# Optimization experiments

Hardware: AMD Instinct MI355X
Metric: run time of the kernel (lower is better)

Reference implementation:

```python
import jax, jax.numpy as jnp
import numpy as np

BS = 128      # batch
L = 512       # encoder sequence length
ENC = 512     # enc_hs
DEC = 1024    # dec_hs
ATTN = 512    # attn_sz
EMB = 256     # emb_sz
VOCAB = 128   # alphabet_size
MAX_LEN = 128 # text_max_len
SOS = 0


def setup_inputs() -> dict:
    key = jax.random.key(0)
    ks = jax.random.split(key, 10)
    s = 0.02
    return {
        "enc_out": jax.random.normal(ks[0], (BS, ENC, L), jnp.float32),
        # attention.encoder_conv (Conv1d enc->attn, kernel 1 == matmul)
        "W_enc": jax.random.normal(ks[1], (ATTN, ENC), jnp.float32) * s,
        "b_enc": jnp.zeros((ATTN,), jnp.float32),
        # attention.decoder_linear
        "W_dec": jax.random.normal(ks[2], (ATTN, DEC), jnp.float32) * s,
        "b_dec": jnp.zeros((ATTN,), jnp.float32),
        # attention.energy_layer (Conv1d attn->1, kernel 1)
        "v_e": jax.random.normal(ks[3], (ATTN,), jnp.float32) * s,
        "b_e": jnp.zeros((), jnp.float32),
        # embedding table
        "emb_table": jax.random.normal(ks[4], (VOCAB, EMB), jnp.float32) * s,
        # LSTM (single layer), PyTorch gate order i,f,g,o
        "W_ih": jax.random.normal(ks[5], (4 * DEC, EMB + ENC), jnp.float32) * s,
        "W_hh": jax.random.normal(ks[6], (4 * DEC, DEC), jnp.float32) * s,
        "b_ih": jnp.zeros((4 * DEC,), jnp.float32),
        "b_hh": jnp.zeros((4 * DEC,), jnp.float32),
        # output projection
        "W_out": jax.random.normal(ks[7], (VOCAB, DEC), jnp.float32) * s,
        "b_out": jnp.zeros((VOCAB,), jnp.float32),
    }


def reference(enc_out, W_enc, b_enc, W_dec, b_dec, v_e, b_e, emb_table,
              W_ih, W_hh, b_ih, b_hh, W_out, b_out):
    bs = enc_out.shape[0]
    # encoder_conv applied once: [bs, attn, L]
    weighted_enc = jnp.einsum('ae,bel->bal', W_enc, enc_out) + b_enc[None, :, None]

    def step(carry, _):
        x_idx, h, c = carry
        emb_x = emb_table[x_idx]                                   # [bs, emb]
        # Bahdanau attention
        wdec = h @ W_dec.T + b_dec                                 # [bs, attn]
        pre = jnp.tanh(weighted_enc + wdec[:, :, None])            # [bs, attn, L]
        scores = jnp.einsum('bal,a->bl', pre, v_e) + b_e           # [bs, L]
        alphas = jax.nn.softmax(scores, axis=-1)                   # [bs, L]
        context = jnp.einsum('bel,bl->be', enc_out, alphas)        # [bs, enc]
        # LSTM cell (PyTorch gate order i, f, g, o)
        rnn_x = jnp.concatenate([emb_x, context], axis=1)          # [bs, emb+enc]
        gates = rnn_x @ W_ih.T + b_ih + h @ W_hh.T + b_hh          # [bs, 4*dec]
        i, f, g, o = jnp.split(gates, 4, axis=1)
        i = jax.nn.sigmoid(i); f = jax.nn.sigmoid(f)
        g = jnp.tanh(g); o = jax.nn.sigmoid(o)
        c_new = f * c + i * g
        h_new = o * jnp.tanh(c_new)
        logits = h_new @ W_out.T + b_out                           # [bs, vocab]
        logp = jax.nn.log_softmax(logits, axis=-1)
        next_word = jnp.argmax(logp, axis=1).astype(jnp.int32)
        return (next_word, h_new, c_new), (logp, next_word, alphas)

    x0 = jnp.full((bs,), SOS, dtype=jnp.int32)
    h0 = jnp.zeros((bs, DEC), enc_out.dtype)
    c0 = jnp.zeros((bs, DEC), enc_out.dtype)
    _, (logp, preds, attn) = jax.lax.scan(step, (x0, h0, c0), None, length=MAX_LEN)
    # [T,bs,*] -> [bs,T,*]
    return logp.transpose(1, 0, 2), preds.transpose(1, 0), attn.transpose(1, 0, 2)
```

## Files before the change

### kernel.cpp

```cpp
#include <hip/hip_runtime.h>
#include <math.h>

#define BS 128
#define L 512
#define ENC 512
#define DEC 1024
#define ATTN 512
#define EMB 256
#define VOCAB 128
#define TMAX 128
#define KCAT 1792
#define G4 4096

#define OFF_WET    0ull
#define OFF_WGR    33554432ull
#define OFF_BGR    40894464ull
#define OFF_WOUTT  40898560ull
#define OFF_WDT    41029632ull
#define OFF_C      41553920ull
#define OFF_XCAT   41816064ull
#define OFF_GPART  42045440ull

__device__ __forceinline__ float tanh_fast(float x) {
    float ax = fabsf(x);
    float e = __expf(-2.f * ax);
    float d = 1.f + e;
    float r = __builtin_amdgcn_rcpf(d);
    r = r * (2.f - d * r);
    float t = 1.f - 2.f * e * r;
    return copysignf(t, x);
}

__global__ void k_prep(const float* __restrict__ W_ih, const float* __restrict__ W_hh,
                       const float* __restrict__ b_ih, const float* __restrict__ b_hh,
                       const float* __restrict__ W_out, const float* __restrict__ W_dec,
                       float* __restrict__ Wgr, float* __restrict__ bgr,
                       float* __restrict__ WoutT, float* __restrict__ WdT) {
    long i = (long)blockIdx.x * 256 + threadIdx.x;
    if (i < (long)G4 * KCAT) {
        int mp = (int)(i / KCAT), k = (int)(i % KCAT);
        int d = mp >> 2, g = mp & 3;
        int r = g * DEC + d;
        Wgr[i] = (k < EMB + ENC) ? W_ih[(long)r * (EMB + ENC) + k]
                                 : W_hh[(long)r * DEC + (k - (EMB + ENC))];
        return;
    }
    long j = i - (long)G4 * KCAT;
    if (j < G4) {
        int d = (int)(j >> 2), g = (int)(j & 3);
        int r = g * DEC + d;
        bgr[j] = b_ih[r] + b_hh[r];
        return;
    }
    long m = j - G4;
    if (m < (long)DEC * VOCAB) {
        int k = (int)(m / VOCAB), v = (int)(m % VOCAB);
        WoutT[m] = W_out[(long)v * DEC + k];
        return;
    }
    long p = m - (long)DEC * VOCAB;
    if (p < (long)DEC * ATTN) {
        int k = (int)(p / ATTN), a = (int)(p % ATTN);
        WdT[p] = W_dec[(long)a * DEC + k];
    }
}

__global__ void k_init(const float* __restrict__ emb_table,
                       float* __restrict__ c, float* __restrict__ Xcat) {
    long i = (long)blockIdx.x * 256 + threadIdx.x;
    if (i < BS * DEC) { c[i] = 0.f; return; }
    long j = i - BS * DEC;
    if (j < (long)BS * KCAT) {
        int cdx = (int)(j % KCAT);
        Xcat[j] = (cdx < EMB) ? emb_table[cdx] : 0.f;
    }
}

__global__ __launch_bounds__(256) void k_wenc(const float* __restrict__ W_enc,
                                              const float* __restrict__ b_enc,
                                              const float* __restrict__ enc_out,
                                              float* __restrict__ weT) {
    __shared__ float As[16][68];
    __shared__ float Bs[16][68];
    int b = blockIdx.z;
    int a0 = blockIdx.y * 64;
    int l0 = blockIdx.x * 64;
    int t = threadIdx.x;
    int ty = t >> 4, tx = t & 15;
    float acc[4][4] = {};
    for (int e0 = 0; e0 < ENC; e0 += 16) {
        {
            int ar = t >> 2;
            int kg = (t & 3) << 2;
            float4 w4 = *(const float4*)&W_enc[(size_t)(a0 + ar) * ENC + e0 + kg];
            As[kg + 0][ar] = w4.x; As[kg + 1][ar] = w4.y; As[kg + 2][ar] = w4.z; As[kg + 3][ar] = w4.w;
            int er = t >> 4;
            int lg = (t & 15) << 2;
            float4 x4 = *(const float4*)&enc_out[((size_t)b * ENC + e0 + er) * L + l0 + lg];
            *(float4*)&Bs[er][lg] = x4;
        }
        __syncthreads();
        #pragma unroll
        for (int kk = 0; kk < 16; kk++) {
            float4 a4 = *(const float4*)&As[kk][ty * 4];
            float4 x4 = *(const float4*)&Bs[kk][tx * 4];
            float av[4] = {a4.x, a4.y, a4.z, a4.w};
            float xv[4] = {x4.x, x4.y, x4.z, x4.w};
            #pragma unroll
            for (int i = 0; i < 4; i++)
                #pragma unroll
                for (int j = 0; j < 4; j++) acc[i][j] += av[i] * xv[j];
        }
        __syncthreads();
    }
    float be0 = b_enc[a0 + ty * 4 + 0];
    float be1 = b_enc[a0 + ty * 4 + 1];
    float be2 = b_enc[a0 + ty * 4 + 2];
    float be3 = b_enc[a0 + ty * 4 + 3];
    #pragma unroll
    for (int j = 0; j < 4; j++) {
        int l = l0 + tx * 4 + j;
        float4 o = {acc[0][j] + be0, acc[1][j] + be1, acc[2][j] + be2, acc[3][j] + be3};
        *(float4*)&weT[((size_t)b * L + l) * ATTN + a0 + ty * 4] = o;
    }
}

__global__ __launch_bounds__(512) void k_ao(const float* __restrict__ gpart,
                                            const float* __restrict__ bgr,
                                            const float* __restrict__ WoutT,
                                            const float* __restrict__ b_out,
                                            const float* __restrict__ emb_table,
                                            const float* __restrict__ WdT,
                                            const float* __restrict__ b_dec,
                                            float* __restrict__ c,
                                            float* __restrict__ logp_out,
                                            float* __restrict__ preds_out,
                                            float* __restrict__ Xcat,
                                            const float* __restrict__ weT,
                                            const float* __restrict__ v_e,
                                            const float* __restrict__ b_e,
                                            const float* __restrict__ enc_out,
                                            float* __restrict__ attn_out, int ts) {
    __shared__ float hs[DEC];
    __shared__ float wd[ATTN];
    __shared__ float ve[ATTN];
    __shared__ float al[L];
    __shared__ float red[512];
    __shared__ float rv[128];
    __shared__ int ri[128];
    int b = blockIdx.x;
    int t = threadIdx.x;

    if (ts > 0) {
        #pragma unroll
        for (int q = 0; q < 2; q++) {
            int d = q * 512 + t;
            const float* gp = gpart + (size_t)b * G4 + d * 4;
            float4 g = *(const float4*)gp;
            #pragma unroll
            for (int ks = 1; ks < 4; ks++) {
                float4 p = *(const float4*)(gp + (size_t)ks * BS * G4);
                g.x += p.x; g.y += p.y; g.z += p.z; g.w += p.w;
            }
            float4 bb = *(const float4*)&bgr[(size_t)d * 4];
            float gi = g.x + bb.x, gf = g.y + bb.y, gg = g.z + bb.z, go = g.w + bb.w;
            float fi = 1.f / (1.f + expf(-gi));
            float ff = 1.f / (1.f + expf(-gf));
            float fg = tanhf(gg);
            float fo = 1.f / (1.f + expf(-go));
            size_t ix = (size_t)b * DEC + d;
            float cn = ff * c[ix] + fi * fg;
            float hn = fo * tanhf(cn);
            c[ix] = cn;
            hs[d] = hn;
            Xcat[(size_t)b * KCAT + EMB + ENC + d] = hn;
        }
        __syncthreads();
        int v = t & 127, kh = t >> 7;
        const float* wp = WoutT + (size_t)kh * 256 * VOCAB + v;
        float acc = 0.f;
        #pragma unroll 8
        for (int k = 0; k < 256; k++) acc += wp[(size_t)k * VOCAB] * hs[kh * 256 + k];
        red[t] = acc;
        __syncthreads();
        float logits = 0.f;
        if (t < 128) {
            logits = ((red[t] + red[t + 128]) + (red[t + 256] + red[t + 384])) + b_out[t];
            rv[t] = logits; ri[t] = t;
        }
        __syncthreads();
        for (int s = 64; s; s >>= 1) {
            if (t < s) {
                float ov = rv[t + s]; int oi = ri[t + s];
                if (ov > rv[t] || (ov == rv[t] && oi < ri[t])) { rv[t] = ov; ri[t] = oi; }
            }
            __syncthreads();
        }
        float m = rv[0]; int am = ri[0];
        __syncthreads();
        if (t < 128) red[t] = expf(logits - m);
        __syncthreads();
        for (int s = 64; s; s >>= 1) { if (t < s && t + s < 128) red[t] += red[t + s]; __syncthreads(); }
        if (t < 128) logp_out[((size_t)b * TMAX + (ts - 1)) * VOCAB + t] = logits - m - logf(red[0]);
        if (t == 0) preds_out[(size_t)b * TMAX + (ts - 1)] = (float)am;
        if (t < 256) Xcat[(size_t)b * KCAT + t] = emb_table[(size_t)am * EMB + t];
        {
            const float* wdp = WdT + t;
            float s = 0.f;
            #pragma unroll 16
            for (int k = 0; k < DEC; k++) s += wdp[(size_t)k * ATTN] * hs[k];
            wd[t] = s + b_dec[t];
        }
        if (ts == TMAX) return;
    } else {
        wd[t] = b_dec[t];
    }
    ve[t] = v_e[t];
    __syncthreads();

    const float* row = weT + ((size_t)b * L + t) * ATTN;
    float acc = 0.f;
    #pragma unroll 8
    for (int a4 = 0; a4 < ATTN; a4 += 4) {
        float4 x = *(const float4*)&row[a4];
        acc += ve[a4 + 0] * tanh_fast(x.x + wd[a4 + 0]);
        acc += ve[a4 + 1] * tanh_fast(x.y + wd[a4 + 1]);
        acc += ve[a4 + 2] * tanh_fast(x.z + wd[a4 + 2]);
        acc += ve[a4 + 3] * tanh_fast(x.w + wd[a4 + 3]);
    }
    float sc = acc + b_e[0];
    red[t] = sc;
    __syncthreads();
    for (int s = 256; s; s >>= 1) { if (t < s) red[t] = fmaxf(red[t], red[t + s]); __syncthreads(); }
    float m = red[0];
    __syncthreads();
    float e = expf(sc - m);
    red[t] = e;
    __syncthreads();
    for (int s = 256; s; s >>= 1) { if (t < s) red[t] += red[t + s]; __syncthreads(); }
    float inv = 1.f / red[0];
    al[t] = e * inv;
    __syncthreads();
    attn_out[((size_t)b * TMAX + ts) * L + t] = al[t];
    const float* erow = enc_out + ((size_t)b * ENC + t) * L;
    float cacc = 0.f;
    #pragma unroll 8
    for (int l4 = 0; l4 < L; l4 += 4) {
        float4 x = *(const float4*)&erow[l4];
        float4 a4 = *(const float4*)&al[l4];
        cacc += x.x * a4.x + x.y * a4.y + x.z * a4.z + x.w * a4.w;
    }
    Xcat[(size_t)b * KCAT + EMB + t] = cacc;
}

__global__ __launch_bounds__(256) void k_gates(const float* __restrict__ Wgr,
                                               const float* __restrict__ Xcat,
                                               float* __restrict__ gates_part) {
    __shared__ float As[16][68];
    __shared__ float Xs[16][36];
    int M0 = blockIdx.x * 64;
    int b0 = blockIdx.y * 32;
    int ks = blockIdx.z;
    int kbase = ks * 448, kend = kbase + 448;
    int t = threadIdx.x, ty = t >> 4, tx = t & 15;
    int r = t >> 2, kg = (t & 3) << 2;
    float acc[4][2] = {};
    float4 wreg = *(const float4*)&Wgr[(size_t)(M0 + r) * KCAT + kbase + kg];
    float4 xreg;
    if (t < 128) xreg = *(const float4*)&Xcat[(size_t)(b0 + r) * KCAT + kbase + kg];
    for (int k0 = kbase; k0 < kend; k0 += 16) {
        As[kg + 0][r] = wreg.x; As[kg + 1][r] = wreg.y; As[kg + 2][r] = wreg.z; As[kg + 3][r] = wreg.w;
        if (t < 128) {
            Xs[kg + 0][r] = xreg.x; Xs[kg + 1][r] = xreg.y; Xs[kg + 2][r] = xreg.z; Xs[kg + 3][r] = xreg.w;
        }
        __syncthreads();
        if (k0 + 16 < kend) {
            wreg = *(const float4*)&Wgr[(size_t)(M0 + r) * KCAT + k0 + 16 + kg];
            if (t < 128) xreg = *(const float4*)&Xcat[(size_t)(b0 + r) * KCAT + k0 + 16 + kg];
        }
        #pragma unroll
        for (int kk = 0; kk < 16; kk++) {
            float4 a4 = *(const float4*)&As[kk][ty * 4];
            float xb0 = Xs[kk][tx * 2], xb1 = Xs[kk][tx * 2 + 1];
            acc[0][0] += a4.x * xb0; acc[0][1] += a4.x * xb1;
            acc[1][0] += a4.y * xb0; acc[1][1] += a4.y * xb1;
            acc[2][0] += a4.z * xb0; acc[2][1] += a4.z * xb1;
            acc[3][0] += a4.w * xb0; acc[3][1] += a4.w * xb1;
        }
        __syncthreads();
    }
    float* gp = gates_part + (size_t)ks * BS * G4;
    #pragma unroll
    for (int j = 0; j < 2; j++) {
        float4 o = {acc[0][j], acc[1][j], acc[2][j], acc[3][j]};
        *(float4*)&gp[(size_t)(b0 + tx * 2 + j) * G4 + M0 + ty * 4] = o;
    }
}

extern "C" void kernel_launch(void* const* d_in, const int* in_sizes, int n_in,
                              void* d_out, int out_size, void* d_ws, size_t ws_size,
                              hipStream_t stream) {
    const float* enc_out = (const float*)d_in[0];
    const float* W_enc   = (const float*)d_in[1];
    const float* b_enc   = (const float*)d_in[2];
    const float* W_dec   = (const float*)d_in[3];
    const float* b_dec   = (const float*)d_in[4];
    const float* v_e     = (const float*)d_in[5];
    const float* b_e     = (const float*)d_in[6];
    const float* emb     = (const float*)d_in[7];
    const float* W_ih    = (const float*)d_in[8];
    const float* W_hh    = (const float*)d_in[9];
    const float* b_ih    = (const float*)d_in[10];
    const float* b_hh    = (const float*)d_in[11];
    const float* W_out   = (const float*)d_in[12];
    const float* b_out   = (const float*)d_in[13];

    float* ws    = (float*)d_ws;
    float* weT   = ws + OFF_WET;
    float* Wgr   = ws + OFF_WGR;
    float* bgr   = ws + OFF_BGR;
    float* WoutT = ws + OFF_WOUTT;
    float* WdT   = ws + OFF_WDT;
    float* c     = ws + OFF_C;
    float* Xcat  = ws + OFF_XCAT;
    float* gpart = ws + OFF_GPART;

    float* logp_out  = (float*)d_out;
    float* preds_out = logp_out + (size_t)BS * TMAX * VOCAB;
    float* attn_out  = preds_out + (size_t)BS * TMAX;

    {
        long n = (long)G4 * KCAT + G4 + (long)DEC * VOCAB + (long)DEC * ATTN;
        k_prep<<<(int)((n + 255) / 256), 256, 0, stream>>>(W_ih, W_hh, b_ih, b_hh, W_out, W_dec,
                                                           Wgr, bgr, WoutT, WdT);
    }
    {
        long n = (long)BS * DEC + (long)BS * KCAT;
        k_init<<<(int)((n + 255) / 256), 256, 0, stream>>>(emb, c, Xcat);
    }
    k_wenc<<<dim3(8, 8, 128), 256, 0, stream>>>(W_enc, b_enc, enc_out, weT);

    for (int t = 0; t < TMAX; t++) {
        k_ao<<<128, 512, 0, stream>>>(gpart, bgr, WoutT, b_out, emb, WdT, b_dec, c,
                                      logp_out, preds_out, Xcat, weT, v_e, b_e,
                                      enc_out, attn_out, t);
        k_gates<<<dim3(64, 4, 4), 256, 0, stream>>>(Wgr, Xcat, gpart);
    }
    k_ao<<<128, 512, 0, stream>>>(gpart, bgr, WoutT, b_out, emb, WdT, b_dec, c,
                                  logp_out, preds_out, Xcat, weT, v_e, b_e,
                                  enc_out, attn_out, TMAX);
}
```

Measured before the change: 22.07 ms.

## Split per-batch attention step across two blocks with pairwise global-flag sync

The per-step attention/output kernel now launches two blocks per batch row instead of one. Each block computes half of the attention scores and half of the context vector, exchanging scores through global memory. The two blocks coordinate with an atomic counter spin barrier, and the old cell state is read before the first barrier so one block can overwrite it safely. The aim is to double the number of active CUs during the memory-bound attention phase, at the cost of redundant LSTM/W_dec work in both blocks and inter-block spin synchronisation that assumes co-residency.

```diff
diff --git a/kernel.cpp b/kernel.cpp
--- a/kernel.cpp
+++ b/kernel.cpp
@@ -18,6 +18,8 @@
 #define OFF_WOUTT  40898560ull
 #define OFF_WDT    41029632ull
 #define OFF_C      41553920ull
+#define OFF_SC     41684992ull
+#define OFF_FLAG   41750528ull
 #define OFF_XCAT   41816064ull
 #define OFF_GPART  42045440ull
 
@@ -29,6 +31,19 @@
     r = r * (2.f - d * r);
     float t = 1.f - 2.f * e * r;
     return copysignf(t, x);
+}
+
+__device__ __forceinline__ void pairsync(int* flag, int target) {
+    __syncthreads();
+    if (threadIdx.x == 0) {
+        __threadfence();
+        __hip_atomic_fetch_add(flag, 1, __ATOMIC_ACQ_REL, __HIP_MEMORY_SCOPE_AGENT);
+        while (__hip_atomic_load(flag, __ATOMIC_RELAXED, __HIP_MEMORY_SCOPE_AGENT) < target) {
+            __builtin_amdgcn_s_sleep(4);
+        }
+        __threadfence();
+    }
+    __syncthreads();
 }
 
 __global__ void k_prep(const float* __restrict__ W_ih, const float* __restrict__ W_hh,
@@ -66,8 +81,10 @@
 }
 
 __global__ void k_init(const float* __restrict__ emb_table,
-                       float* __restrict__ c, float* __restrict__ Xcat) {
+                       float* __restrict__ c, float* __restrict__ Xcat,
+                       int* __restrict__ flags) {
     long i = (long)blockIdx.x * 256 + threadIdx.x;
+    if (i < BS * 16) flags[i] = 0;
     if (i < BS * DEC) { c[i] = 0.f; return; }
     long j = i - BS * DEC;
     if (j < (long)BS * KCAT) {
@@ -125,22 +142,24 @@
     }
 }
 
-__global__ __launch_bounds__(512) void k_ao(const float* __restrict__ gpart,
-                                            const float* __restrict__ bgr,
-                                            const float* __restrict__ WoutT,
-                                            const float* __restrict__ b_out,
-                                            const float* __restrict__ emb_table,
-                                            const float* __restrict__ WdT,
-                                            const float* __restrict__ b_dec,
-                                            float* __restrict__ c,
-                                            float* __restrict__ logp_out,
-                                            float* __restrict__ preds_out,
-                                            float* __restrict__ Xcat,
-                                            const float* __restrict__ weT,
-                                            const float* __restrict__ v_e,
-                                            const float* __restrict__ b_e,
-                                            const float* __restrict__ enc_out,
-                                            float* __restrict__ attn_out, int ts) {
+__global__ __launch_bounds__(512) void k_aof(const float* __restrict__ gpart,
+                                             const float* __restrict__ bgr,
+                                             const float* __restrict__ WoutT,
+                                             const float* __restrict__ b_out,
+                                             const float* __restrict__ emb_table,
+                                             const float* __restrict__ WdT,
+                                             const float* __restrict__ b_dec,
+                                             float* __restrict__ c,
+                                             float* __restrict__ logp_out,
+                                             float* __restrict__ preds_out,
+                                             float* __restrict__ Xcat,
+                                             const float* __restrict__ weT,
+                                             const float* __restrict__ v_e,
+                                             const float* __restrict__ b_e,
+                                             const float* __restrict__ enc_out,
+                                             float* __restrict__ attn_out,
+                                             float* __restrict__ sc_g,
+                                             int* __restrict__ flags, int ts) {
     __shared__ float hs[DEC];
     __shared__ float wd[ATTN];
     __shared__ float ve[ATTN];
@@ -148,10 +167,16 @@
     __shared__ float red[512];
     __shared__ float rv[128];
     __shared__ int ri[128];
-    int b = blockIdx.x;
+    __shared__ float scl[256];
+    int b = blockIdx.x >> 1, h = blockIdx.x & 1;
     int t = threadIdx.x;
+    int* flag = flags + b * 16;
+    int msync = (ts == 0) ? 0 : (2 * ts - 1);
 
     if (ts > 0) {
+        float cold0 = c[(size_t)b * DEC + t];
+        float cold1 = c[(size_t)b * DEC + 512 + t];
+        pairsync(flag, 2 * (++msync));
         #pragma unroll
         for (int q = 0; q < 2; q++) {
             int d = q * 512 + t;
@@ -168,42 +193,46 @@
             float ff = 1.f / (1.f + expf(-gf));
             float fg = tanhf(gg);
             float fo = 1.f / (1.f + expf(-go));
-            size_t ix = (size_t)b * DEC + d;
-            float cn = ff * c[ix] + fi * fg;
+            float cold = q ? cold1 : cold0;
+            float cn = ff * cold + fi * fg;
             float hn = fo * tanhf(cn);
-            c[ix] = cn;
+            if (h == 0) {
+                c[(size_t)b * DEC + d] = cn;
+                Xcat[(size_t)b * KCAT + EMB + ENC + d] = hn;
+            }
             hs[d] = hn;
-            Xcat[(size_t)b * KCAT + EMB + ENC + d] = hn;
         }
         __syncthreads();
-        int v = t & 127, kh = t >> 7;
-        const float* wp = WoutT + (size_t)kh * 256 * VOCAB + v;
-        float acc = 0.f;
-        #pragma unroll 8
-        for (int k = 0; k < 256; k++) acc += wp[(size_t)k * VOCAB] * hs[kh * 256 + k];
-        red[t] = acc;
-        __syncthreads();
-        float logits = 0.f;
-        if (t < 128) {
-            logits = ((red[t] + red[t + 128]) + (red[t + 256] + red[t + 384])) + b_out[t];
-            rv[t] = logits; ri[t] = t;
-        }
-        __syncthreads();
-        for (int s = 64; s; s >>= 1) {
-            if (t < s) {
-                float ov = rv[t + s]; int oi = ri[t + s];
-                if (ov > rv[t] || (ov == rv[t] && oi < ri[t])) { rv[t] = ov; ri[t] = oi; }
+        if (h == 0) {
+            int v = t & 127, kh = t >> 7;
+            const float* wp = WoutT + (size_t)kh * 256 * VOCAB + v;
+            float acc = 0.f;
+            #pragma unroll 8
+            for (int k = 0; k < 256; k++) acc += wp[(size_t)k * VOCAB] * hs[kh * 256 + k];
+            red[t] = acc;
+            __syncthreads();
+            float logits = 0.f;
+            if (t < 128) {
+                logits = ((red[t] + red[t + 128]) + (red[t + 256] + red[t + 384])) + b_out[t];
+                rv[t] = logits; ri[t] = t;
             }
             __syncthreads();
-        }
-        float m = rv[0]; int am = ri[0];
-        __syncthreads();
-        if (t < 128) red[t] = expf(logits - m);
-        __syncthreads();
-        for (int s = 64; s; s >>= 1) { if (t < s && t + s < 128) red[t] += red[t + s]; __syncthreads(); }
-        if (t < 128) logp_out[((size_t)b * TMAX + (ts - 1)) * VOCAB + t] = logits - m - logf(red[0]);
-        if (t == 0) preds_out[(size_t)b * TMAX + (ts - 1)] = (float)am;
-        if (t < 256) Xcat[(size_t)b * KCAT + t] = emb_table[(size_t)am * EMB + t];
+            for (int s = 64; s; s >>= 1) {
+                if (t < s) {
+                    float ov = rv[t + s]; int oi = ri[t + s];
+                    if (ov > rv[t] || (ov == rv[t] && oi < ri[t])) { rv[t] = ov; ri[t] = oi; }
+                }
+                __syncthreads();
+            }
+            float m = rv[0]; int am = ri[0];
+            __syncthreads();
+            if (t < 128) red[t] = expf(logits - m);
+            __syncthreads();
+            for (int s = 64; s; s >>= 1) { if (t < s && t + s < 128) red[t] += red[t + s]; __syncthreads(); }
+            if (t < 128) logp_out[((size_t)b * TMAX + (ts - 1)) * VOCAB + t] = logits - m - logf(red[0]);
+            if (t == 0) preds_out[(size_t)b * TMAX + (ts - 1)] = (float)am;
+            if (t < 256) Xcat[(size_t)b * KCAT + t] = emb_table[(size_t)am * EMB + t];
+        }
         {
             const float* wdp = WdT + t;
             float s = 0.f;
@@ -218,17 +247,32 @@
     ve[t] = v_e[t];
     __syncthreads();
 
-    const float* row = weT + ((size_t)b * L + t) * ATTN;
-    float acc = 0.f;
-    #pragma unroll 8
-    for (int a4 = 0; a4 < ATTN; a4 += 4) {
-        float4 x = *(const float4*)&row[a4];
-        acc += ve[a4 + 0] * tanh_fast(x.x + wd[a4 + 0]);
-        acc += ve[a4 + 1] * tanh_fast(x.y + wd[a4 + 1]);
-        acc += ve[a4 + 2] * tanh_fast(x.z + wd[a4 + 2]);
-        acc += ve[a4 + 3] * tanh_fast(x.w + wd[a4 + 3]);
-    }
-    float sc = acc + b_e[0];
+    {
+        int r2 = t >> 1, ah = t & 1;
+        int l = h * 256 + r2;
+        const float* row = weT + ((size_t)b * L + l) * ATTN + ah * 256;
+        float acc = 0.f;
+        #pragma unroll 8
+        for (int a4 = 0; a4 < 256; a4 += 4) {
+            float4 x = *(const float4*)&row[a4];
+            int a = ah * 256 + a4;
+            acc += ve[a + 0] * tanh_fast(x.x + wd[a + 0]);
+            acc += ve[a + 1] * tanh_fast(x.y + wd[a + 1]);
+            acc += ve[a + 2] * tanh_fast(x.z + wd[a + 2]);
+            acc += ve[a + 3] * tanh_fast(x.w + wd[a + 3]);
+        }
+        acc += __shfl_xor(acc, 1, 64);
+        if (ah == 0) {
+            float s = acc + b_e[0];
+            scl[r2] = s;
+            sc_g[(size_t)b * L + l] = s;
+        }
+    }
+    pairsync(flag, 2 * (++msync));
+
+    float sc;
+    if (t >= h * 256 && t < h * 256 + 256) sc = scl[t - h * 256];
+    else sc = sc_g[(size_t)b * L + t];
     red[t] = sc;
     __syncthreads();
     for (int s = 256; s; s >>= 1) { if (t < s) red[t] = fmaxf(red[t], red[t + s]); __syncthreads(); }
@@ -241,16 +285,22 @@
     float inv = 1.f / red[0];
     al[t] = e * inv;
     __syncthreads();
-    attn_out[((size_t)b * TMAX + ts) * L + t] = al[t];
-    const float* erow = enc_out + ((size_t)b * ENC + t) * L;
-    float cacc = 0.f;
-    #pragma unroll 8
-    for (int l4 = 0; l4 < L; l4 += 4) {
-        float4 x = *(const float4*)&erow[l4];
-        float4 a4 = *(const float4*)&al[l4];
-        cacc += x.x * a4.x + x.y * a4.y + x.z * a4.z + x.w * a4.w;
-    }
-    Xcat[(size_t)b * KCAT + EMB + t] = cacc;
+    if (h == 0) attn_out[((size_t)b * TMAX + ts) * L + t] = al[t];
+
+    {
+        int r2 = t >> 1, lh2 = (t & 1) * 256;
+        int e_ = h * 256 + r2;
+        const float* erow = enc_out + ((size_t)b * ENC + e_) * L + lh2;
+        float cacc = 0.f;
+        #pragma unroll 8
+        for (int l4 = 0; l4 < 256; l4 += 4) {
+            float4 x = *(const float4*)&erow[l4];
+            float4 a4 = *(const float4*)&al[lh2 + l4];
+            cacc += x.x * a4.x + x.y * a4.y + x.z * a4.z + x.w * a4.w;
+        }
+        cacc += __shfl_xor(cacc, 1, 64);
+        if ((t & 1) == 0) Xcat[(size_t)b * KCAT + EMB + e_] = cacc;
+    }
 }
 
 __global__ __launch_bounds__(256) void k_gates(const float* __restrict__ Wgr,
@@ -322,6 +372,8 @@
     float* WoutT = ws + OFF_WOUTT;
     float* WdT   = ws + OFF_WDT;
     float* c     = ws + OFF_C;
+    float* sc_g  = ws + OFF_SC;
+    int*   flags = (int*)(ws + OFF_FLAG);
     float* Xcat  = ws + OFF_XCAT;
     float* gpart = ws + OFF_GPART;
 
@@ -336,17 +388,17 @@
     }
     {
         long n = (long)BS * DEC + (long)BS * KCAT;
-        k_init<<<(int)((n + 255) / 256), 256, 0, stream>>>(emb, c, Xcat);
+        k_init<<<(int)((n + 255) / 256), 256, 0, stream>>>(emb, c, Xcat, flags);
     }
     k_wenc<<<dim3(8, 8, 128), 256, 0, stream>>>(W_enc, b_enc, enc_out, weT);
 
     for (int t = 0; t < TMAX; t++) {
-        k_ao<<<128, 512, 0, stream>>>(gpart, bgr, WoutT, b_out, emb, WdT, b_dec, c,
-                                      logp_out, preds_out, Xcat, weT, v_e, b_e,
-                                      enc_out, attn_out, t);
+        k_aof<<<256, 512, 0, stream>>>(gpart, bgr, WoutT, b_out, emb, WdT, b_dec, c,
+                                       logp_out, preds_out, Xcat, weT, v_e, b_e,
+                                       enc_out, attn_out, sc_g, flags, t);
         k_gates<<<dim3(64, 4, 4), 256, 0, stream>>>(Wgr, Xcat, gpart);
     }
-    k_ao<<<128, 512, 0, stream>>>(gpart, bgr, WoutT, b_out, emb, WdT, b_dec, c,
-                                  logp_out, preds_out, Xcat, weT, v_e, b_e,
-                                  enc_out, attn_out, TMAX);
-}
+    k_aof<<<256, 512, 0, stream>>>(gpart, bgr, WoutT, b_out, emb, WdT, b_dec, c,
+                                   logp_out, preds_out, Xcat, weT, v_e, b_e,
+                                   enc_out, attn_out, sc_g, flags, TMAX);
+}
```

Result: faster. 20.49 ms (-7.2%).
